# Kernel tuning notes

Hardware: AMD Instinct MI355X
Metric: run time of the kernel (lower is better)

## Reference

```python
import jax, jax.numpy as jnp
import numpy as np

B, C, H, W = 16, 256, 64, 64
CI = 128  # inter_channels = in_channels // 2
BN_EPS = 1e-5


def _conv1x1(t, w, b):
    # 1x1 conv: t [B,Cin,H,W], w [Cout,Cin], b [Cout]
    return jnp.einsum('bchw,dc->bdhw', t, w) + b[None, :, None, None]


def _maxpool2(t):
    # 2x2 max pool, stride 2: [B,C,H,W] -> [B,C,H/2,W/2]
    b, c, h, w = t.shape
    return t.reshape(b, c, h // 2, 2, w // 2, 2).max(axis=(3, 5))


def setup_inputs() -> dict:
    key = jax.random.key(0)
    ks = jax.random.split(key, 8)
    s = lambda k, shape: (jax.random.normal(k, shape, jnp.float32) * 0.05)
    return {
        'x': jax.random.normal(ks[0], (B, C, H, W), jnp.float32),
        'theta_w': s(ks[1], (CI, C)), 'theta_b': s(ks[2], (CI,)),
        'phi_w': s(ks[3], (CI, C)), 'phi_b': s(ks[4], (CI,)),
        'g_w': s(ks[5], (CI, C)), 'g_b': s(ks[6], (CI,)),
        'W_w': s(ks[7], (C, CI)), 'W_b': jnp.zeros((C,), jnp.float32),
        'bn_gamma': jnp.ones((C,), jnp.float32),
        'bn_beta': jnp.zeros((C,), jnp.float32),
    }


def reference(x, theta_w, theta_b, phi_w, phi_b, g_w, g_b, W_w, W_b, bn_gamma, bn_beta):
    b, c, h, w = x.shape
    ci = theta_w.shape[0]
    # theta (query): [B, N, Ci], N = H*W
    theta_x = _conv1x1(x, theta_w, theta_b).reshape(b, ci, h * w).transpose(0, 2, 1)
    # phi (key), sub-sampled: [B, Ci, M], M = H*W/4
    phi_x = _maxpool2(_conv1x1(x, phi_w, phi_b)).reshape(b, ci, -1)
    # g (value), sub-sampled: [B, M, Ci]
    g_x = _maxpool2(_conv1x1(x, g_w, g_b)).reshape(b, ci, -1).transpose(0, 2, 1)
    # affinity [B, N, M], normalized by number of key positions (f.size(-1))
    f_div_C = jnp.einsum('bnc,bcm->bnm', theta_x, phi_x) / phi_x.shape[-1]
    # weighted aggregation: [B, N, Ci]
    y = jnp.einsum('bnm,bmc->bnc', f_div_C, g_x)
    y = y.transpose(0, 2, 1).reshape(b, ci, h, w)
    # output projection (1x1 conv) + BatchNorm (training-mode batch stats)
    w_y = _conv1x1(y, W_w, W_b)
    mean = w_y.mean(axis=(0, 2, 3), keepdims=True)
    var = w_y.var(axis=(0, 2, 3), keepdims=True)
    w_y = (w_y - mean) * jax.lax.rsqrt(var + BN_EPS)
    w_y = w_y * bn_gamma[None, :, None, None] + bn_beta[None, :, None, None]
    return w_y + x
```

## Files before the change

### kernel.cpp

```cpp
#include <hip/hip_runtime.h>

#define DEVI static __device__ __forceinline__

typedef __attribute__((ext_vector_type(8))) short bf16x8;
typedef __attribute__((ext_vector_type(4))) float f32x4;

DEVI ushort f2bf(float f) {
  union { float f; unsigned u; } v; v.f = f;
  unsigned r = v.u + 0x7fffu + ((v.u >> 16) & 1u);
  return (ushort)(r >> 16);
}
DEVI float bf2f(ushort u) {
  union { unsigned u; float f; } v; v.u = ((unsigned)u) << 16;
  return v.f;
}

#define WS_XT    0ull
#define WS_WCAT  33554432ull
#define WS_RST   33554432ull
#define WS_S     35651584ull
#define WS_SUM   35667968ull
#define WS_WY    35672064ull
#define WS_PHI   WS_WY
#define WS_G     (WS_WY + 8388608ull)
#define WS_PG    (WS_WY + 16777216ull)

__global__ __launch_bounds__(256) void kprep(
    const float* __restrict__ x, const float* __restrict__ phw,
    const float* __restrict__ gww, char* __restrict__ ws) {
  __shared__ float tile[64 * 65];
  const int bid = blockIdx.x, t = threadIdx.x;
  if (bid < 4096) {
    const int b = bid >> 8, rem = bid & 255;
    const int c0 = (rem >> 6) * 64, n0 = (rem & 63) * 64;
    const float* xb = x + ((size_t)(b * 256 + c0)) * 4096 + n0;
#pragma unroll
    for (int it = 0; it < 4; ++it) {
      int ch = t + it * 256;
      int cr = ch >> 4, nf = ch & 15;
      float4 v = *(const float4*)(xb + (size_t)cr * 4096 + nf * 4);
      tile[cr * 65 + nf * 4 + 0] = v.x;
      tile[cr * 65 + nf * 4 + 1] = v.y;
      tile[cr * 65 + nf * 4 + 2] = v.z;
      tile[cr * 65 + nf * 4 + 3] = v.w;
    }
    __syncthreads();
    ushort* xT = (ushort*)(ws + WS_XT);
#pragma unroll
    for (int it = 0; it < 2; ++it) {
      int ch = t + it * 256;
      int rn = ch >> 3, jc = ch & 7;
      uint4 pk;
      pk.x = (unsigned)f2bf(tile[(jc * 8 + 0) * 65 + rn]) | ((unsigned)f2bf(tile[(jc * 8 + 1) * 65 + rn]) << 16);
      pk.y = (unsigned)f2bf(tile[(jc * 8 + 2) * 65 + rn]) | ((unsigned)f2bf(tile[(jc * 8 + 3) * 65 + rn]) << 16);
      pk.z = (unsigned)f2bf(tile[(jc * 8 + 4) * 65 + rn]) | ((unsigned)f2bf(tile[(jc * 8 + 5) * 65 + rn]) << 16);
      pk.w = (unsigned)f2bf(tile[(jc * 8 + 6) * 65 + rn]) | ((unsigned)f2bf(tile[(jc * 8 + 7) * 65 + rn]) << 16);
      *(uint4*)(xT + ((size_t)(b * 4096 + n0 + rn)) * 256 + c0 + jc * 8) = pk;
    }
  } else if (bid == 4096) {
    ushort* Wcat = (ushort*)(ws + WS_WCAT);
    for (int idx = t; idx < 65536; idx += 256) {
      int ci = idx >> 8, c = idx & 255;
      float v = (ci < 128) ? phw[ci * 256 + c] : gww[(ci - 128) * 256 + c];
      Wcat[idx] = f2bf(v);
    }
  } else {
    float4 z = {0.f, 0.f, 0.f, 0.f};
    float4* st = (float4*)(ws + WS_SUM);
    if (t < 128) st[t] = z;
  }
}

__global__ __launch_bounds__(256) void kconvpg(
    const float* __restrict__ phib, const float* __restrict__ gb,
    char* __restrict__ ws) {
  __shared__ __align__(16) char lds[49152];
  const int t = threadIdx.x;
  const int b = blockIdx.y, nb = blockIdx.x;
  const int n0 = nb * 128;
  const int lane = t & 63, wave = t >> 6;
  const int lr = lane & 15, lq = lane >> 4;
  const ushort* xT = (const ushort*)(ws + WS_XT) + ((size_t)(b * 4096 + n0)) * 256;
  const ushort* Wc = (const ushort*)(ws + WS_WCAT);

  f32x4 acc[8][4];
#pragma unroll
  for (int i = 0; i < 8; ++i)
#pragma unroll
    for (int j = 0; j < 4; ++j) acc[i][j] = (f32x4){0.f, 0.f, 0.f, 0.f};

  int4 ra[4], rb[8];
#pragma unroll
  for (int it = 0; it < 4; ++it) {
    int ch = t + it * 256, r = ch >> 3, jc = ch & 7;
    ra[it] = *(const int4*)(xT + (size_t)r * 256 + jc * 8);
  }
#pragma unroll
  for (int it = 0; it < 8; ++it) {
    int ch = t + it * 256, r = ch >> 3, jc = ch & 7;
    rb[it] = *(const int4*)(Wc + r * 256 + jc * 8);
  }
  const int swz = (lr & 7) << 4;

  for (int ks = 0; ks < 4; ++ks) {
#pragma unroll
    for (int it = 0; it < 4; ++it) {
      int ch = t + it * 256, r = ch >> 3, jc = ch & 7;
      *(int4*)(lds + r * 128 + ((jc * 16) ^ ((r & 7) << 4))) = ra[it];
    }
#pragma unroll
    for (int it = 0; it < 8; ++it) {
      int ch = t + it * 256, r = ch >> 3, jc = ch & 7;
      *(int4*)(lds + 16384 + r * 128 + ((jc * 16) ^ ((r & 7) << 4))) = rb[it];
    }
    __syncthreads();
    if (ks < 3) {
#pragma unroll
      for (int it = 0; it < 4; ++it) {
        int ch = t + it * 256, r = ch >> 3, jc = ch & 7;
        ra[it] = *(const int4*)(xT + (size_t)r * 256 + (ks + 1) * 64 + jc * 8);
      }
#pragma unroll
      for (int it = 0; it < 8; ++it) {
        int ch = t + it * 256, r = ch >> 3, jc = ch & 7;
        rb[it] = *(const int4*)(Wc + r * 256 + (ks + 1) * 64 + jc * 8);
      }
    }
#pragma unroll
    for (int k2 = 0; k2 < 2; ++k2) {
      const int kb = k2 * 64 + lq * 16;
      bf16x8 bfr[4];
#pragma unroll
      for (int j = 0; j < 4; ++j) {
        int bc = wave * 64 + j * 16 + lr;
        bfr[j] = *(const bf16x8*)(lds + 16384 + bc * 128 + (kb ^ swz));
      }
#pragma unroll
      for (int i = 0; i < 8; ++i) {
        int arw = i * 16 + lr;
        bf16x8 af = *(const bf16x8*)(lds + arw * 128 + (kb ^ swz));
#pragma unroll
        for (int j = 0; j < 4; ++j)
          acc[i][j] = __builtin_amdgcn_mfma_f32_16x16x32_bf16(af, bfr[j], acc[i][j], 0, 0, 0);
      }
    }
    __syncthreads();
  }
  float* pool = (float*)lds;
#pragma unroll
  for (int j = 0; j < 4; ++j) {
    int cir = wave * 64 + j * 16 + lr;
    float bias = (cir < 128) ? phib[cir] : gb[cir - 128];
#pragma unroll
    for (int i = 0; i < 4; ++i) {
      f32x4 lo = acc[i][j], hi = acc[i + 4][j];
      float m0 = fmaxf(fmaxf(lo[0], lo[1]), fmaxf(hi[0], hi[1])) + bias;
      float m1 = fmaxf(fmaxf(lo[2], lo[3]), fmaxf(hi[2], hi[3])) + bias;
      pool[cir * 36 + i * 8 + lq * 2] = m0;
      pool[cir * 36 + i * 8 + lq * 2 + 1] = m1;
    }
  }
  __syncthreads();
  const int rr_ = t >> 3, chk = t & 7;
#pragma unroll
  for (int pass = 0; pass < 8; ++pass) {
    int ci = pass * 32 + rr_;
    float4 v = *(const float4*)(pool + ci * 36 + chk * 4);
    float* dst = (ci < 128)
        ? ((float*)(ws + WS_PHI) + ((size_t)(b * 128 + ci)) * 1024)
        : ((float*)(ws + WS_G) + ((size_t)(b * 128 + ci - 128)) * 1024);
    *(float4*)(dst + nb * 32 + chk * 4) = v;
  }
}

__global__ __launch_bounds__(256) void kpg32(char* __restrict__ ws) {
  __shared__ float lphi[32 * 65];
  __shared__ float lgd[32 * 65];
  const int t = threadIdx.x, b = blockIdx.y, kz = blockIdx.z;
  const int cib = blockIdx.x >> 2, cjb = blockIdx.x & 3;
  const int ci_l = t >> 5, cj_l = t & 31;
  const float* phi = (const float*)(ws + WS_PHI) + ((size_t)(b * 128 + cib * 32)) * 1024;
  const float* gg = (const float*)(ws + WS_G) + ((size_t)(b * 128 + cjb * 32)) * 1024;
  float acc[4] = {0.f, 0.f, 0.f, 0.f};
  for (int kc = kz * 4; kc < kz * 4 + 4; ++kc) {
#pragma unroll
    for (int it = 0; it < 8; ++it) {
      int fi = t + it * 256;
      int r = fi >> 6, c = fi & 63;
      lphi[r * 65 + c] = phi[(size_t)r * 1024 + kc * 64 + c];
      lgd[r * 65 + c] = gg[(size_t)r * 1024 + kc * 64 + c];
    }
    __syncthreads();
#pragma unroll 8
    for (int k = 0; k < 64; ++k) {
      float gv = lgd[cj_l * 65 + k];
#pragma unroll
      for (int p = 0; p < 4; ++p)
        acc[p] += lphi[(ci_l * 4 + p) * 65 + k] * gv;
    }
    __syncthreads();
  }
  float* PG = (float*)(ws + WS_PG) + (size_t)kz * 262144 + (size_t)b * 16384;
#pragma unroll
  for (int p = 0; p < 4; ++p)
    PG[(cib * 32 + ci_l * 4 + p) * 128 + cjb * 32 + cj_l] = acc[p];
}

__global__ __launch_bounds__(256) void kmid(
    const float* __restrict__ thw, const float* __restrict__ thb,
    const float* __restrict__ wbias, const float* __restrict__ www,
    char* __restrict__ ws) {
  __shared__ __align__(16) char smid[49920];
  float* PGc = (float*)smid;
  float* Wws = (float*)(smid + 16896);
  float* Qts = (float*)(smid + 33408);
  float* thws = (float*)smid;
  const int t = threadIdx.x, b = blockIdx.y, cblk = blockIdx.x;
  const int c_l = t >> 3, q = t & 7;
  const float* PG0 = (const float*)(ws + WS_PG) + (size_t)b * 16384;

#pragma unroll
  for (int it = 0; it < 16; ++it) {
    int fi = t + it * 256;
    int r = fi >> 7, j = fi & 127;
    Wws[r * 129 + j] = www[(cblk * 32 + r) * 128 + j];
  }
  float qacc[16];
#pragma unroll
  for (int i = 0; i < 16; ++i) qacc[i] = 0.f;

  for (int jc = 0; jc < 4; ++jc) {
#pragma unroll
    for (int it = 0; it < 16; ++it) {
      int fi = t + it * 256;
      int i = fi >> 5, jl = fi & 31;
      int idx = i * 128 + jc * 32 + jl;
      PGc[i * 33 + jl] = PG0[idx] + PG0[262144 + idx] + PG0[524288 + idx] + PG0[786432 + idx];
    }
    __syncthreads();
#pragma unroll
    for (int iq = 0; iq < 16; ++iq) {
      int i = iq * 8 + q;
      float a = 0.f;
#pragma unroll 8
      for (int jl = 0; jl < 32; ++jl)
        a += Wws[c_l * 129 + jc * 32 + jl] * PGc[i * 33 + jl];
      qacc[iq] += a;
    }
    __syncthreads();
  }
  const float inv = 1.0f / 1024.0f;
#pragma unroll
  for (int iq = 0; iq < 16; ++iq) Qts[c_l * 129 + iq * 8 + q] = qacc[iq] * inv;
  __syncthreads();
  if (t < 32) {
    float sv = wbias[cblk * 32 + t];
    for (int i = 0; i < 128; ++i) sv += thb[i] * Qts[t * 129 + i];
    ((float*)(ws + WS_S))[b * 256 + cblk * 32 + t] = sv;
  }
  ushort* Rstb = (ushort*)(ws + WS_RST) + (size_t)b * 65536;
  for (int cpc = 0; cpc < 4; ++cpc) {
#pragma unroll
    for (int it = 0; it < 32; ++it) {
      int fi = t + it * 256;
      int i = fi >> 6, cp = fi & 63;
      thws[i * 65 + cp] = thw[i * 256 + cpc * 64 + cp];
    }
    __syncthreads();
#pragma unroll
    for (int k = 0; k < 8; ++k) {
      int cpl = q * 8 + k;
      float a = 0.f;
#pragma unroll 8
      for (int i = 0; i < 128; ++i)
        a += Qts[c_l * 129 + i] * thws[i * 65 + cpl];
      Rstb[(cblk * 32 + c_l) * 256 + cpc * 64 + cpl] = f2bf(a);
    }
    __syncthreads();
  }
}

__global__ __launch_bounds__(256) void kwyT(char* __restrict__ ws) {
  __shared__ __align__(16) char lds[40960];
  const int t = threadIdx.x;
  const int b = blockIdx.y, nb = blockIdx.x;
  const int n0 = nb * 64;
  const int lane = t & 63, wave = t >> 6;
  const int lr = lane & 15, lq = lane >> 4;
  const ushort* xT = (const ushort*)(ws + WS_XT) + ((size_t)(b * 4096 + n0)) * 256;
  const ushort* Rst = (const ushort*)(ws + WS_RST) + (size_t)b * 65536;

  f32x4 acc[4][4];
#pragma unroll
  for (int i = 0; i < 4; ++i)
#pragma unroll
    for (int j = 0; j < 4; ++j) acc[i][j] = (f32x4){0.f, 0.f, 0.f, 0.f};

  int4 ra[8], rb[2];
#pragma unroll
  for (int it = 0; it < 8; ++it) {
    int ch = t + it * 256, r = ch >> 3, jc = ch & 7;
    ra[it] = *(const int4*)(Rst + r * 256 + jc * 8);
  }
#pragma unroll
  for (int it = 0; it < 2; ++it) {
    int ch = t + it * 256, r = ch >> 3, jc = ch & 7;
    rb[it] = *(const int4*)(xT + (size_t)r * 256 + jc * 8);
  }

  for (int ks = 0; ks < 4; ++ks) {
#pragma unroll
    for (int it = 0; it < 8; ++it) {
      int ch = t + it * 256, r = ch >> 3, jc = ch & 7;
      *(int4*)(lds + r * 128 + ((jc * 16) ^ ((r & 7) << 4))) = ra[it];
    }
#pragma unroll
    for (int it = 0; it < 2; ++it) {
      int ch = t + it * 256, r = ch >> 3, jc = ch & 7;
      *(int4*)(lds + 32768 + r * 128 + ((jc * 16) ^ ((r & 7) << 4))) = rb[it];
    }
    __syncthreads();
    if (ks < 3) {
#pragma unroll
      for (int it = 0; it < 8; ++it) {
        int ch = t + it * 256, r = ch >> 3, jc = ch & 7;
        ra[it] = *(const int4*)(Rst + r * 256 + (ks + 1) * 64 + jc * 8);
      }
#pragma unroll
      for (int it = 0; it < 2; ++it) {
        int ch = t + it * 256, r = ch >> 3, jc = ch & 7;
        rb[it] = *(const int4*)(xT + (size_t)r * 256 + (ks + 1) * 64 + jc * 8);
      }
    }
#pragma unroll
    for (int k2 = 0; k2 < 2; ++k2) {
      const int kb = k2 * 64 + lq * 16;
      bf16x8 bfr[4];
#pragma unroll
      for (int j = 0; j < 4; ++j) {
        int rn = j * 16 + lr;
        bfr[j] = *(const bf16x8*)(lds + 32768 + rn * 128 + (kb ^ ((rn & 7) << 4)));
      }
#pragma unroll
      for (int i = 0; i < 4; ++i) {
        int rc = wave * 64 + i * 16 + lr;
        bf16x8 af = *(const bf16x8*)(lds + rc * 128 + (kb ^ ((rc & 7) << 4)));
#pragma unroll
        for (int j = 0; j < 4; ++j)
          acc[i][j] = __builtin_amdgcn_mfma_f32_16x16x32_bf16(af, bfr[j], acc[i][j], 0, 0, 0);
      }
    }
    __syncthreads();
  }
  ushort* po = (ushort*)lds;
#pragma unroll
  for (int i = 0; i < 4; ++i)
#pragma unroll
    for (int j = 0; j < 4; ++j)
#pragma unroll
      for (int rr = 0; rr < 4; ++rr) {
        int c_ = wave * 64 + i * 16 + lq * 4 + rr;
        po[c_ * 72 + j * 16 + lr] = f2bf(acc[i][j][rr]);
      }
  __syncthreads();
  const float* sarr = (const float*)(ws + WS_S) + b * 256;
  ushort* wyb = (ushort*)(ws + WS_WY) + (size_t)b * 1048576;
  float* sls = (float*)(lds + 36864);
  const int rr_ = t >> 3, chk = t & 7;
#pragma unroll
  for (int pass = 0; pass < 8; ++pass) {
    int c = pass * 32 + rr_;
    int4 v = *(const int4*)(po + c * 72 + chk * 8);
    float sv = sarr[c];
    unsigned w[4] = {(unsigned)v.x, (unsigned)v.y, (unsigned)v.z, (unsigned)v.w};
    float s1 = 0.f, s2 = 0.f;
    unsigned o[4];
#pragma unroll
    for (int q = 0; q < 4; ++q) {
      float f0 = bf2f((ushort)(w[q] & 0xffffu)) + sv;
      float f1 = bf2f((ushort)(w[q] >> 16)) + sv;
      s1 += f0 + f1;
      s2 += f0 * f0 + f1 * f1;
      o[q] = (unsigned)f2bf(f0) | ((unsigned)f2bf(f1) << 16);
    }
    int4 ov;
    ov.x = (int)o[0]; ov.y = (int)o[1]; ov.z = (int)o[2]; ov.w = (int)o[3];
    *(int4*)(wyb + (size_t)c * 4096 + n0 + chk * 8) = ov;
    s1 += __shfl_xor(s1, 1); s1 += __shfl_xor(s1, 2); s1 += __shfl_xor(s1, 4);
    s2 += __shfl_xor(s2, 1); s2 += __shfl_xor(s2, 2); s2 += __shfl_xor(s2, 4);
    if (chk == 0) { sls[c] = s1; sls[256 + c] = s2; }
  }
  __syncthreads();
  float2 pv;
  pv.x = sls[t];
  pv.y = sls[256 + t];
  float2* pslot = (float2*)((ushort*)(ws + WS_XT) + ((size_t)(b * 4096 + n0)) * 256);
  pslot[t] = pv;
}

__global__ __launch_bounds__(256) void kstat(char* __restrict__ ws) {
  const int t = threadIdx.x, blk = blockIdx.x;
  float a1 = 0.f, a2 = 0.f;
  const ushort* xTbase = (const ushort*)(ws + WS_XT);
  for (int i = 0; i < 32; ++i) {
    int s = blk * 32 + i;
    int b = s >> 6, nb = s & 63;
    const float2* p = (const float2*)(xTbase + ((size_t)(b * 4096 + nb * 64)) * 256);
    float2 v = p[t];
    a1 += v.x;
    a2 += v.y;
  }
  float* gsum = (float*)(ws + WS_SUM);
  atomicAdd(&gsum[t], a1);
  atomicAdd(&gsum[256 + t], a2);
}

__global__ __launch_bounds__(256) void kout(
    const float* __restrict__ x, const float* __restrict__ gamma,
    const float* __restrict__ beta, const char* __restrict__ ws,
    float* __restrict__ out) {
  __shared__ float scaleL[256], shiftL[256];
  const int t = threadIdx.x;
  const int b = blockIdx.y, blk = blockIdx.x;
  {
    const float* gsum = (const float*)(ws + WS_SUM);
    float sm = gsum[t], sq = gsum[256 + t];
    float mean = sm * (1.0f / 65536.0f);
    float var = sq * (1.0f / 65536.0f) - mean * mean;
    float rs = rsqrtf(var + 1e-5f);
    float sc = gamma[t] * rs;
    scaleL[t] = sc;
    shiftL[t] = beta[t] - mean * sc;
  }
  __syncthreads();
  const ushort* wyb = (const ushort*)(ws + WS_WY) + (size_t)b * 1048576;
  const float* xb = x + (size_t)b * 1048576;
  float* ob = out + (size_t)b * 1048576;
#pragma unroll
  for (int it = 0; it < 8; ++it) {
    int idx = blk * 8192 + it * 1024 + t * 4;
    int c = idx >> 12;
    uint2 wv = *(const uint2*)(wyb + idx);
    float4 xv = *(const float4*)(xb + idx);
    float sc = scaleL[c], sh = shiftL[c];
    float4 ov;
    ov.x = bf2f((ushort)(wv.x & 0xffffu)) * sc + sh + xv.x;
    ov.y = bf2f((ushort)(wv.x >> 16)) * sc + sh + xv.y;
    ov.z = bf2f((ushort)(wv.y & 0xffffu)) * sc + sh + xv.z;
    ov.w = bf2f((ushort)(wv.y >> 16)) * sc + sh + xv.w;
    *(float4*)(ob + idx) = ov;
  }
}

extern "C" void kernel_launch(void* const* d_in, const int* in_sizes, int n_in,
                              void* d_out, int out_size, void* d_ws, size_t ws_size,
                              hipStream_t stream) {
  const float* x = (const float*)d_in[0];
  const float* thw = (const float*)d_in[1];
  const float* thb = (const float*)d_in[2];
  const float* phw = (const float*)d_in[3];
  const float* phb = (const float*)d_in[4];
  const float* gw = (const float*)d_in[5];
  const float* gb = (const float*)d_in[6];
  const float* www = (const float*)d_in[7];
  const float* wwb = (const float*)d_in[8];
  const float* gamma = (const float*)d_in[9];
  const float* beta = (const float*)d_in[10];
  char* ws = (char*)d_ws;
  float* out = (float*)d_out;

  kprep<<<dim3(4098), dim3(256), 0, stream>>>(x, phw, gw, ws);
  kconvpg<<<dim3(32, 16), dim3(256), 0, stream>>>(phb, gb, ws);
  kpg32<<<dim3(16, 16, 4), dim3(256), 0, stream>>>(ws);
  kmid<<<dim3(8, 16), dim3(256), 0, stream>>>(thw, thb, wwb, www, ws);
  kwyT<<<dim3(64, 16), dim3(256), 0, stream>>>(ws);
  kstat<<<dim3(32), dim3(256), 0, stream>>>(ws);
  kout<<<dim3(128, 16), dim3(256), 0, stream>>>(x, gamma, beta, ws, out);
}
```

Measured before the change: 433.1 us.

## Fuse x transpose and bf16 conversion into GEMM loaders, drop xT buffer

```diff
diff --git a/kernel.cpp b/kernel.cpp
--- a/kernel.cpp
+++ b/kernel.cpp
@@ -15,49 +15,21 @@
   return v.f;
 }
 
-#define WS_XT    0ull
-#define WS_WCAT  33554432ull
-#define WS_RST   33554432ull
-#define WS_S     35651584ull
-#define WS_SUM   35667968ull
-#define WS_WY    35672064ull
+#define WS_WCAT  0ull
+#define WS_RST   131072ull
+#define WS_S     2228224ull
+#define WS_SUM   2244608ull
+#define WS_PART  2246656ull
+#define WS_WY    4343808ull
 #define WS_PHI   WS_WY
 #define WS_G     (WS_WY + 8388608ull)
 #define WS_PG    (WS_WY + 16777216ull)
 
-__global__ __launch_bounds__(256) void kprep(
-    const float* __restrict__ x, const float* __restrict__ phw,
-    const float* __restrict__ gww, char* __restrict__ ws) {
-  __shared__ float tile[64 * 65];
+__global__ __launch_bounds__(256) void kprep2(
+    const float* __restrict__ phw, const float* __restrict__ gww,
+    char* __restrict__ ws) {
   const int bid = blockIdx.x, t = threadIdx.x;
-  if (bid < 4096) {
-    const int b = bid >> 8, rem = bid & 255;
-    const int c0 = (rem >> 6) * 64, n0 = (rem & 63) * 64;
-    const float* xb = x + ((size_t)(b * 256 + c0)) * 4096 + n0;
-#pragma unroll
-    for (int it = 0; it < 4; ++it) {
-      int ch = t + it * 256;
-      int cr = ch >> 4, nf = ch & 15;
-      float4 v = *(const float4*)(xb + (size_t)cr * 4096 + nf * 4);
-      tile[cr * 65 + nf * 4 + 0] = v.x;
-      tile[cr * 65 + nf * 4 + 1] = v.y;
-      tile[cr * 65 + nf * 4 + 2] = v.z;
-      tile[cr * 65 + nf * 4 + 3] = v.w;
-    }
-    __syncthreads();
-    ushort* xT = (ushort*)(ws + WS_XT);
-#pragma unroll
-    for (int it = 0; it < 2; ++it) {
-      int ch = t + it * 256;
-      int rn = ch >> 3, jc = ch & 7;
-      uint4 pk;
-      pk.x = (unsigned)f2bf(tile[(jc * 8 + 0) * 65 + rn]) | ((unsigned)f2bf(tile[(jc * 8 + 1) * 65 + rn]) << 16);
-      pk.y = (unsigned)f2bf(tile[(jc * 8 + 2) * 65 + rn]) | ((unsigned)f2bf(tile[(jc * 8 + 3) * 65 + rn]) << 16);
-      pk.z = (unsigned)f2bf(tile[(jc * 8 + 4) * 65 + rn]) | ((unsigned)f2bf(tile[(jc * 8 + 5) * 65 + rn]) << 16);
-      pk.w = (unsigned)f2bf(tile[(jc * 8 + 6) * 65 + rn]) | ((unsigned)f2bf(tile[(jc * 8 + 7) * 65 + rn]) << 16);
-      *(uint4*)(xT + ((size_t)(b * 4096 + n0 + rn)) * 256 + c0 + jc * 8) = pk;
-    }
-  } else if (bid == 4096) {
+  if (bid == 0) {
     ushort* Wcat = (ushort*)(ws + WS_WCAT);
     for (int idx = t; idx < 65536; idx += 256) {
       int ci = idx >> 8, c = idx & 255;
@@ -72,16 +44,16 @@
 }
 
 __global__ __launch_bounds__(256) void kconvpg(
-    const float* __restrict__ phib, const float* __restrict__ gb,
-    char* __restrict__ ws) {
+    const float* __restrict__ x, const float* __restrict__ phib,
+    const float* __restrict__ gb, char* __restrict__ ws) {
   __shared__ __align__(16) char lds[49152];
   const int t = threadIdx.x;
   const int b = blockIdx.y, nb = blockIdx.x;
   const int n0 = nb * 128;
   const int lane = t & 63, wave = t >> 6;
   const int lr = lane & 15, lq = lane >> 4;
-  const ushort* xT = (const ushort*)(ws + WS_XT) + ((size_t)(b * 4096 + n0)) * 256;
   const ushort* Wc = (const ushort*)(ws + WS_WCAT);
+  const float* xb = x + (size_t)b * 1048576 + n0;
 
   f32x4 acc[8][4];
 #pragma unroll
@@ -89,41 +61,57 @@
 #pragma unroll
     for (int j = 0; j < 4; ++j) acc[i][j] = (f32x4){0.f, 0.f, 0.f, 0.f};
 
-  int4 ra[4], rb[8];
+  float4 av0[4], av1[4];
+  int4 rbv[8];
 #pragma unroll
   for (int it = 0; it < 4; ++it) {
-    int ch = t + it * 256, r = ch >> 3, jc = ch & 7;
-    ra[it] = *(const int4*)(xT + (size_t)r * 256 + jc * 8);
+    int idx = t + it * 256;
+    int p = idx >> 5, q = idx & 31;
+    av0[it] = *(const float4*)(xb + (size_t)(2 * p) * 4096 + q * 4);
+    av1[it] = *(const float4*)(xb + (size_t)(2 * p + 1) * 4096 + q * 4);
   }
 #pragma unroll
   for (int it = 0; it < 8; ++it) {
     int ch = t + it * 256, r = ch >> 3, jc = ch & 7;
-    rb[it] = *(const int4*)(Wc + r * 256 + jc * 8);
+    rbv[it] = *(const int4*)(Wc + r * 256 + jc * 8);
   }
   const int swz = (lr & 7) << 4;
 
   for (int ks = 0; ks < 4; ++ks) {
 #pragma unroll
     for (int it = 0; it < 4; ++it) {
-      int ch = t + it * 256, r = ch >> 3, jc = ch & 7;
-      *(int4*)(lds + r * 128 + ((jc * 16) ^ ((r & 7) << 4))) = ra[it];
+      int idx = t + it * 256;
+      int p = idx >> 5, q = idx & 31;
+      float a0[4] = {av0[it].x, av0[it].y, av0[it].z, av0[it].w};
+      float a1[4] = {av1[it].x, av1[it].y, av1[it].z, av1[it].w};
+#pragma unroll
+      for (int i = 0; i < 4; ++i) {
+        int r = q * 4 + i;
+        unsigned pk = (unsigned)f2bf(a0[i]) | ((unsigned)f2bf(a1[i]) << 16);
+        int off = p * 4;
+        int soff = (off & 15) | ((off & 0x70) ^ ((r & 7) << 4));
+        *(unsigned*)(lds + r * 128 + soff) = pk;
+      }
     }
 #pragma unroll
     for (int it = 0; it < 8; ++it) {
       int ch = t + it * 256, r = ch >> 3, jc = ch & 7;
-      *(int4*)(lds + 16384 + r * 128 + ((jc * 16) ^ ((r & 7) << 4))) = rb[it];
+      *(int4*)(lds + 16384 + r * 128 + ((jc * 16) ^ ((r & 7) << 4))) = rbv[it];
     }
     __syncthreads();
     if (ks < 3) {
+      const float* xn = xb + (size_t)(ks + 1) * 64 * 4096;
 #pragma unroll
       for (int it = 0; it < 4; ++it) {
-        int ch = t + it * 256, r = ch >> 3, jc = ch & 7;
-        ra[it] = *(const int4*)(xT + (size_t)r * 256 + (ks + 1) * 64 + jc * 8);
+        int idx = t + it * 256;
+        int p = idx >> 5, q = idx & 31;
+        av0[it] = *(const float4*)(xn + (size_t)(2 * p) * 4096 + q * 4);
+        av1[it] = *(const float4*)(xn + (size_t)(2 * p + 1) * 4096 + q * 4);
       }
 #pragma unroll
       for (int it = 0; it < 8; ++it) {
         int ch = t + it * 256, r = ch >> 3, jc = ch & 7;
-        rb[it] = *(const int4*)(Wc + r * 256 + (ks + 1) * 64 + jc * 8);
+        rbv[it] = *(const int4*)(Wc + r * 256 + (ks + 1) * 64 + jc * 8);
       }
     }
 #pragma unroll
@@ -280,14 +268,15 @@
   }
 }
 
-__global__ __launch_bounds__(256) void kwyT(char* __restrict__ ws) {
+__global__ __launch_bounds__(256) void kwyS(
+    const float* __restrict__ x, char* __restrict__ ws) {
   __shared__ __align__(16) char lds[40960];
   const int t = threadIdx.x;
   const int b = blockIdx.y, nb = blockIdx.x;
   const int n0 = nb * 64;
   const int lane = t & 63, wave = t >> 6;
   const int lr = lane & 15, lq = lane >> 4;
-  const ushort* xT = (const ushort*)(ws + WS_XT) + ((size_t)(b * 4096 + n0)) * 256;
+  const float* xb = x + (size_t)b * 1048576 + n0;
   const ushort* Rst = (const ushort*)(ws + WS_RST) + (size_t)b * 65536;
 
   f32x4 acc[4][4];
@@ -296,7 +285,8 @@
 #pragma unroll
     for (int j = 0; j < 4; ++j) acc[i][j] = (f32x4){0.f, 0.f, 0.f, 0.f};
 
-  int4 ra[8], rb[2];
+  int4 ra[8];
+  float4 xv0[2], xv1[2];
 #pragma unroll
   for (int it = 0; it < 8; ++it) {
     int ch = t + it * 256, r = ch >> 3, jc = ch & 7;
@@ -304,8 +294,10 @@
   }
 #pragma unroll
   for (int it = 0; it < 2; ++it) {
-    int ch = t + it * 256, r = ch >> 3, jc = ch & 7;
-    rb[it] = *(const int4*)(xT + (size_t)r * 256 + jc * 8);
+    int idx = t + it * 256;
+    int p = idx >> 4, q = idx & 15;
+    xv0[it] = *(const float4*)(xb + (size_t)(2 * p) * 4096 + q * 4);
+    xv1[it] = *(const float4*)(xb + (size_t)(2 * p + 1) * 4096 + q * 4);
   }
 
   for (int ks = 0; ks < 4; ++ks) {
@@ -316,11 +308,22 @@
     }
 #pragma unroll
     for (int it = 0; it < 2; ++it) {
-      int ch = t + it * 256, r = ch >> 3, jc = ch & 7;
-      *(int4*)(lds + 32768 + r * 128 + ((jc * 16) ^ ((r & 7) << 4))) = rb[it];
+      int idx = t + it * 256;
+      int p = idx >> 4, q = idx & 15;
+      float a0[4] = {xv0[it].x, xv0[it].y, xv0[it].z, xv0[it].w};
+      float a1[4] = {xv1[it].x, xv1[it].y, xv1[it].z, xv1[it].w};
+#pragma unroll
+      for (int i = 0; i < 4; ++i) {
+        int r = q * 4 + i;
+        unsigned pk = (unsigned)f2bf(a0[i]) | ((unsigned)f2bf(a1[i]) << 16);
+        int off = p * 4;
+        int soff = (off & 15) | ((off & 0x70) ^ ((r & 7) << 4));
+        *(unsigned*)(lds + 32768 + r * 128 + soff) = pk;
+      }
     }
     __syncthreads();
     if (ks < 3) {
+      const float* xn = xb + (size_t)(ks + 1) * 64 * 4096;
 #pragma unroll
       for (int it = 0; it < 8; ++it) {
         int ch = t + it * 256, r = ch >> 3, jc = ch & 7;
@@ -328,8 +331,10 @@
       }
 #pragma unroll
       for (int it = 0; it < 2; ++it) {
-        int ch = t + it * 256, r = ch >> 3, jc = ch & 7;
-        rb[it] = *(const int4*)(xT + (size_t)r * 256 + (ks + 1) * 64 + jc * 8);
+        int idx = t + it * 256;
+        int p = idx >> 4, q = idx & 15;
+        xv0[it] = *(const float4*)(xn + (size_t)(2 * p) * 4096 + q * 4);
+        xv1[it] = *(const float4*)(xn + (size_t)(2 * p + 1) * 4096 + q * 4);
       }
     }
 #pragma unroll
@@ -394,18 +399,15 @@
   float2 pv;
   pv.x = sls[t];
   pv.y = sls[256 + t];
-  float2* pslot = (float2*)((ushort*)(ws + WS_XT) + ((size_t)(b * 4096 + n0)) * 256);
+  float2* pslot = (float2*)(ws + WS_PART) + (size_t)(b * 64 + nb) * 256;
   pslot[t] = pv;
 }
 
 __global__ __launch_bounds__(256) void kstat(char* __restrict__ ws) {
   const int t = threadIdx.x, blk = blockIdx.x;
   float a1 = 0.f, a2 = 0.f;
-  const ushort* xTbase = (const ushort*)(ws + WS_XT);
   for (int i = 0; i < 32; ++i) {
-    int s = blk * 32 + i;
-    int b = s >> 6, nb = s & 63;
-    const float2* p = (const float2*)(xTbase + ((size_t)(b * 4096 + nb * 64)) * 256);
+    const float2* p = (const float2*)(ws + WS_PART) + (size_t)(blk * 32 + i) * 256;
     float2 v = p[t];
     a1 += v.x;
     a2 += v.y;
@@ -469,11 +471,11 @@
   char* ws = (char*)d_ws;
   float* out = (float*)d_out;
 
-  kprep<<<dim3(4098), dim3(256), 0, stream>>>(x, phw, gw, ws);
-  kconvpg<<<dim3(32, 16), dim3(256), 0, stream>>>(phb, gb, ws);
+  kprep2<<<dim3(2), dim3(256), 0, stream>>>(phw, gw, ws);
+  kconvpg<<<dim3(32, 16), dim3(256), 0, stream>>>(x, phb, gb, ws);
   kpg32<<<dim3(16, 16, 4), dim3(256), 0, stream>>>(ws);
   kmid<<<dim3(8, 16), dim3(256), 0, stream>>>(thw, thb, wwb, www, ws);
-  kwyT<<<dim3(64, 16), dim3(256), 0, stream>>>(ws);
+  kwyS<<<dim3(64, 16), dim3(256), 0, stream>>>(x, ws);
   kstat<<<dim3(32), dim3(256), 0, stream>>>(ws);
   kout<<<dim3(128, 16), dim3(256), 0, stream>>>(x, gamma, beta, ws, out);
 }
```

Result: faster. 374.4 us (-13.6%).
